# Kernel optimization log

Measured on AMD Instinct MI355X. Metric: run time of the kernel, lower is better.

Reference implementation:

```python
import jax, jax.numpy as jnp
import numpy as np

NA = 5            # num_anchors
NC = 13           # num_classes
COORD_SCALE = 1.0
NOOBJ_SCALE = 1.0
OBJ_SCALE = 5.0
# corner_confidence9 constants (singleshotpose defaults)
TH = 80.0
SHARP = 2.0
IMW = 640.0
IMH = 480.0


def _forward(output, target):
    nB, _, nH, nW = output.shape
    out = output.reshape(nB, NA, 19 + NC, nH, nW)
    # channels 0,1 sigmoided in-place in the torch code; 2..17 raw
    xys_pred = jnp.concatenate([jax.nn.sigmoid(out[:, :, 0:2]), out[:, :, 2:18]], axis=2)  # [nB,nA,18,nH,nW]
    conf = jax.nn.sigmoid(out[:, :, 18])  # [nB,nA,nH,nW]

    # --- build_targets (done on output.data / target.data in torch -> stop_gradient) ---
    pc = jax.lax.stop_gradient(xys_pred)
    gxr = jnp.arange(nW, dtype=pc.dtype)
    gyr = jnp.arange(nH, dtype=pc.dtype)
    px = (pc[:, :, 0::2] + gxr[None, None, None, None, :]) / nW  # [nB,nA,9,nH,nW] normalized x corners
    py = (pc[:, :, 1::2] + gyr[None, None, None, :, None]) / nH  # [nB,nA,9,nH,nW] normalized y corners

    tgt = jax.lax.stop_gradient(target).reshape(nB, 50, 21)
    coords = tgt[:, :, 1:19]  # [nB,50,18] normalized gt corners (x0,y0,...,x8,y8)
    # torch loop breaks at first zero x0 -> prefix-valid mask
    valid = jnp.cumprod((coords[:, :, 0] != 0).astype(jnp.int32), axis=1).astype(bool)
    gi = jnp.floor(coords[:, :, 0] * nW).astype(jnp.int32)  # [nB,50]
    gj = jnp.floor(coords[:, :, 1] * nH).astype(jnp.int32)

    b_idx = jnp.broadcast_to(jnp.arange(nB)[:, None], (nB, 50))
    # predicted box at assigned cell, anchor best_n = 0 (as in source)
    prx = px[b_idx, 0, :, gj, gi]  # [nB,50,9]
    pry = py[b_idx, 0, :, gj, gi]
    pbox = jnp.stack([prx, pry], axis=-1).reshape(nB, 50, 18)

    # corner_confidence9 (singleshotpose): mean of thresholded exp-distance conf over 9 corners
    d = (coords - pbox).reshape(nB, 50, 9, 2) * jnp.array([IMW, IMH], dtype=coords.dtype)
    dn = jnp.sqrt(jnp.sum(d * d, axis=-1))  # [nB,50,9] pixel distances
    cvals = (jnp.exp(SHARP * (1.0 - dn / TH)) - 1.0) * (dn < TH).astype(coords.dtype)
    conf_t = jnp.mean(cvals, axis=-1) / (jnp.exp(jnp.asarray(SHARP, coords.dtype)) - 1.0 + 1e-5)  # [nB,50]

    # route invalid targets out of bounds -> dropped by scatter
    gi_s = jnp.where(valid, gi, nW)
    gj_s = jnp.where(valid, gj, nH)
    bf = b_idx.reshape(-1)
    gif = gi_s.reshape(-1)
    gjf = gj_s.reshape(-1)

    coord_mask = jnp.zeros((nB, NA, nH, nW), output.dtype).at[bf, 0, gjf, gif].set(1.0)
    conf_mask = jnp.full((nB, NA, nH, nW), NOOBJ_SCALE, output.dtype).at[bf, 0, gjf, gif].set(OBJ_SCALE)
    tconf = jnp.zeros((nB, NA, nH, nW), output.dtype).at[bf, 0, gjf, gif].set(conf_t.reshape(-1))

    tx = coords[:, :, 0::2] * nW - gi[..., None].astype(coords.dtype)  # [nB,50,9]
    ty = coords[:, :, 1::2] * nH - gj[..., None].astype(coords.dtype)
    tvals = jnp.stack([tx, ty], axis=-1).reshape(nB * 50, 18)
    tar = jnp.zeros((nB, NA, 18, nH, nW), output.dtype).at[bf, 0, :, gjf, gif].set(tvals)

    # --- losses ---
    cm = coord_mask[:, :, None]  # [nB,nA,1,nH,nW]
    loss_xy = COORD_SCALE * jnp.sum((xys_pred * cm - tar * cm) ** 2) / 2.0
    cms = jnp.sqrt(conf_mask)
    loss_conf = jnp.sum((conf * cms - tconf * cms) ** 2) / 2.0
    return loss_xy + loss_conf


def setup_inputs() -> dict:
    key = jax.random.key(0)
    k1, k2 = jax.random.split(key)
    output = jax.random.normal(k1, (32, NA * (19 + NC), 76, 76), dtype=jnp.float32)
    target = jax.random.uniform(k2, (32, 50 * 21), dtype=jnp.float32)
    return {"output": output, "target": target}


def reference(output, target):
    return _forward(output, target)
```

## Files before the change

### kernel.cpp

```cpp
#include <hip/hip_runtime.h>
#include <math.h>

#define NB 32
#define NA 5
#define NC 13
#define NHH 76
#define NWW 76
#define NT 50
#define CH (19 + NC)
#define CELLS (NHH * NWW)
#define NBA (NB * NA)
#define V4_PER_SLAB (CELLS / 4)
#define TOTAL_V4 (NBA * V4_PER_SLAB)
#define SWEEP_BLOCKS 192
#define GRID_BLOCKS (SWEEP_BLOCKS + NB)

#define OBJ_SCALE 5.0f
#define TH_ 80.0f
#define SHARP_ 2.0f
#define IMW_ 640.0f
#define IMH_ 480.0f

__device__ __forceinline__ float sigmoidf_(float x) {
    return 1.0f / (1.0f + expf(-x));
}

__global__ void main_kernel(const float* __restrict__ outp,
                            const float* __restrict__ tgt,
                            float* __restrict__ out) {
    int bid = blockIdx.x;
    int tid = threadIdx.x;
    double local = 0.0;

    if (bid < SWEEP_BLOCKS) {
        for (int idx = bid * 256 + tid; idx < TOTAL_V4; idx += SWEEP_BLOCKS * 256) {
            int ba = idx / V4_PER_SLAB;
            int r  = idx - ba * V4_PER_SLAB;
            const float4* slab =
                (const float4*)(outp + ((size_t)ba * CH + 18) * CELLS);
            float4 q = slab[r];
            float a0 = sigmoidf_(q.x), a1 = sigmoidf_(q.y);
            float a2 = sigmoidf_(q.z), a3 = sigmoidf_(q.w);
            local += 0.5 * (double)(a0 * a0 + a1 * a1 + a2 * a2 + a3 * a3);
        }
    } else {
        int b = bid - SWEEP_BLOCKS;
        __shared__ int sgi[NT], sgj[NT], snz[NT], svalid[NT];

        if (tid < NT) {
            const float* tg = tgt + (size_t)(b * NT + tid) * 21;
            float cx = tg[1];
            float cy = tg[2];
            sgi[tid] = (int)floorf(cx * (float)NWW);
            sgj[tid] = (int)floorf(cy * (float)NHH);
            snz[tid] = (cx != 0.0f) ? 1 : 0;
        }
        __syncthreads();
        if (tid < NT) {
            int v = 1;
            for (int k = 0; k <= tid; ++k) v &= snz[k];
            svalid[tid] = v;
        }
        __syncthreads();

        if (tid < NT) {
            int gi = sgi[tid], gj = sgj[tid];
            bool inb = (gi >= 0 && gi < NWW && gj >= 0 && gj < NHH);
            bool win = svalid[tid] && inb;
            if (win) {
                for (int k2 = tid + 1; k2 < NT; ++k2) {
                    if (svalid[k2] && sgi[k2] == gi && sgj[k2] == gj) { win = false; break; }
                }
            }
            if (win) {
                const float* tg = tgt + (size_t)(b * NT + tid) * 21;
                int cell = gj * NWW + gi;
                const float* base = outp + (size_t)b * NA * CH * CELLS;

                float v[19];
                #pragma unroll
                for (int c = 0; c < 19; ++c) v[c] = base[(size_t)c * CELLS + cell];
                float s0 = sigmoidf_(v[0]);
                float s1 = sigmoidf_(v[1]);
                float confv = sigmoidf_(v[18]);

                const float denom = expf(SHARP_) - 1.0f + 1e-5f;
                float ssum = 0.0f;
                #pragma unroll
                for (int k = 0; k < 9; ++k) {
                    float vx = (k == 0) ? s0 : v[2 * k];
                    float vy = (k == 0) ? s1 : v[2 * k + 1];
                    float px = (vx + (float)gi) / (float)NWW;
                    float py = (vy + (float)gj) / (float)NHH;
                    float dx = (tg[1 + 2 * k] - px) * IMW_;
                    float dy = (tg[2 + 2 * k] - py) * IMH_;
                    float dn = sqrtf(dx * dx + dy * dy);
                    if (dn < TH_) ssum += expf(SHARP_ * (1.0f - dn / TH_)) - 1.0f;
                }
                float conf_t = (ssum / 9.0f) / denom;

                float cs = 0.0f;
                #pragma unroll
                for (int k = 0; k < 9; ++k) {
                    float tvx = tg[1 + 2 * k] * (float)NWW - (float)gi;
                    float tvy = tg[2 + 2 * k] * (float)NHH - (float)gj;
                    float dx = ((k == 0) ? s0 : v[2 * k]) - tvx;
                    float dy = ((k == 0) ? s1 : v[2 * k + 1]) - tvy;
                    cs += dx * dx + dy * dy;
                }

                float dc = confv - conf_t;
                local = 0.5 * (double)(OBJ_SCALE * dc * dc - confv * confv + cs);
            }
        }
    }

    __shared__ double sdata[256];
    sdata[tid] = local;
    __syncthreads();
    for (int s = 128; s > 0; s >>= 1) {
        if (tid < s) sdata[tid] += sdata[tid + s];
        __syncthreads();
    }
    if (tid == 0) atomicAdd(out, (float)sdata[0]);
}

extern "C" void kernel_launch(void* const* d_in, const int* in_sizes, int n_in,
                              void* d_out, int out_size, void* d_ws, size_t ws_size,
                              hipStream_t stream) {
    const float* outp = (const float*)d_in[0];
    const float* tgt  = (const float*)d_in[1];
    float* out = (float*)d_out;

    hipMemsetAsync(out, 0, sizeof(float), stream);
    main_kernel<<<GRID_BLOCKS, 256, 0, stream>>>(outp, tgt, out);
}
```

Measured before the change: 22.44 us.

## Drop memset launch via self-resetting workspace accumulator and last-block finalize

Removes the separate hipMemsetAsync on the output. Instead, blocks atomically add a double partial into a workspace accumulator and bump a counter; the last block to arrive writes the total and resets both to a poison pattern, so the next call starts from a known state. The counter check accepts either a zero or a poison starting value. The sweep now gives each block one full confidence slab rather than a grid-stride loop over 192 blocks. The cost is extra per-block atomics and reliance on state persisting in the workspace across calls; the poison bits left in the accumulator decode to a tiny nonzero double.

```diff
diff --git a/kernel.cpp b/kernel.cpp
--- a/kernel.cpp
+++ b/kernel.cpp
@@ -11,8 +11,7 @@
 #define CELLS (NHH * NWW)
 #define NBA (NB * NA)
 #define V4_PER_SLAB (CELLS / 4)
-#define TOTAL_V4 (NBA * V4_PER_SLAB)
-#define SWEEP_BLOCKS 192
+#define SWEEP_BLOCKS NBA
 #define GRID_BLOCKS (SWEEP_BLOCKS + NB)
 
 #define OBJ_SCALE 5.0f
@@ -21,23 +20,24 @@
 #define IMW_ 640.0f
 #define IMH_ 480.0f
 
+#define POISON64 0xAAAAAAAAAAAAAAAAull
+
 __device__ __forceinline__ float sigmoidf_(float x) {
     return 1.0f / (1.0f + expf(-x));
 }
 
 __global__ void main_kernel(const float* __restrict__ outp,
                             const float* __restrict__ tgt,
+                            unsigned long long* __restrict__ ws64,
                             float* __restrict__ out) {
     int bid = blockIdx.x;
     int tid = threadIdx.x;
     double local = 0.0;
 
     if (bid < SWEEP_BLOCKS) {
-        for (int idx = bid * 256 + tid; idx < TOTAL_V4; idx += SWEEP_BLOCKS * 256) {
-            int ba = idx / V4_PER_SLAB;
-            int r  = idx - ba * V4_PER_SLAB;
-            const float4* slab =
-                (const float4*)(outp + ((size_t)ba * CH + 18) * CELLS);
+        const float4* slab =
+            (const float4*)(outp + ((size_t)bid * CH + 18) * CELLS);
+        for (int r = tid; r < V4_PER_SLAB; r += 256) {
             float4 q = slab[r];
             float a0 = sigmoidf_(q.x), a1 = sigmoidf_(q.y);
             float a2 = sigmoidf_(q.z), a3 = sigmoidf_(q.w);
@@ -122,7 +122,25 @@
         if (tid < s) sdata[tid] += sdata[tid + s];
         __syncthreads();
     }
-    if (tid == 0) atomicAdd(out, (float)sdata[0]);
+
+    if (tid == 0) {
+        double* acc = (double*)&ws64[0];
+        unsigned long long* cnt = &ws64[1];
+
+        double old_acc = atomicAdd(acc, sdata[0]);
+        asm volatile("" : : "v"(old_acc));
+        asm volatile("s_waitcnt vmcnt(0)" ::: "memory");
+
+        unsigned long long oc = atomicAdd(cnt, 1ull);
+
+        if (oc == (unsigned long long)(GRID_BLOCKS - 1) ||
+            oc == POISON64 + (unsigned long long)(GRID_BLOCKS - 1)) {
+            unsigned long long bits = atomicExch(&ws64[0], POISON64);
+            double total = __longlong_as_double(bits);
+            out[0] = (float)total;
+            atomicExch(cnt, POISON64);
+        }
+    }
 }
 
 extern "C" void kernel_launch(void* const* d_in, const int* in_sizes, int n_in,
@@ -131,7 +149,7 @@
     const float* outp = (const float*)d_in[0];
     const float* tgt  = (const float*)d_in[1];
     float* out = (float*)d_out;
+    unsigned long long* ws64 = (unsigned long long*)d_ws;
 
-    hipMemsetAsync(out, 0, sizeof(float), stream);
-    main_kernel<<<GRID_BLOCKS, 256, 0, stream>>>(outp, tgt, out);
+    main_kernel<<<GRID_BLOCKS, 256, 0, stream>>>(outp, tgt, ws64, out);
 }
```

After: 18.82 us (median of 2 runs). 16.1% less time.
